# Performance work log

Measured on AMD Instinct MI355X. Metric: run time of the kernel, lower is better.

The kernel has to match this reference:

```python
import jax, jax.numpy as jnp
import numpy as np

N_NODES = 100000


def _gcn_layer(h, W, b, src, dst, norm, n):
    # h: [N, Fin] -> [N, Fout]; normalized scatter-add aggregation (GCNConv)
    hw = h @ W
    msg = norm[:, None] * hw[src]
    out = jax.ops.segment_sum(msg, dst, num_segments=n)
    return out + b


def setup_inputs() -> dict:
    key = jax.random.key(0)
    k = jax.random.split(key, 10)
    N, E, P, F = N_NODES, 3200000, 500000, 128
    x = jax.random.normal(k[0], (N, F), dtype=jnp.float32)
    edge_index = jax.random.randint(k[1], (2, E), 0, N, dtype=jnp.int64)
    pred_edges = jax.random.randint(k[2], (P, 2), 0, N, dtype=jnp.int64)
    # Glorot-ish init for learned params
    W1 = jax.random.normal(k[3], (F, 16), dtype=jnp.float32) / np.sqrt(F)
    b1 = jnp.zeros((16,), dtype=jnp.float32)
    W2 = jax.random.normal(k[4], (16, 8), dtype=jnp.float32) / np.sqrt(16.0)
    b2 = jnp.zeros((8,), dtype=jnp.float32)
    Wl = jax.random.normal(k[5], (8, 1), dtype=jnp.float32) / np.sqrt(8.0)
    bl = jnp.zeros((1,), dtype=jnp.float32)
    return {"x": x, "edge_index": edge_index, "pred_edges": pred_edges,
            "W1": W1, "b1": b1, "W2": W2, "b2": b2, "Wl": Wl, "bl": bl}


def reference(x, edge_index, pred_edges, W1, b1, W2, b2, Wl, bl):
    n = x.shape[0]
    # GCN norm with self-loops: A_hat = D^{-1/2}(A+I)D^{-1/2}
    loop = jnp.arange(n, dtype=edge_index.dtype)
    src = jnp.concatenate([edge_index[0], loop])
    dst = jnp.concatenate([edge_index[1], loop])
    deg = jax.ops.segment_sum(jnp.ones_like(dst, dtype=x.dtype), dst, num_segments=n)
    dinv = jnp.where(deg > 0, jax.lax.rsqrt(deg), 0.0)
    norm = dinv[src] * dinv[dst]

    h = _gcn_layer(x, W1, b1, src, dst, norm, n)   # [N, 16]
    h = _gcn_layer(h, W2, b2, src, dst, norm, n)   # [N, 8]
    z = jax.nn.sigmoid(h @ Wl + bl)                # [N, 1]
    m = z[pred_edges]                              # [P, 2, 1]
    pred = m[:, 0, 0] * m[:, 1, 0]                 # [P]
    return pred
```

## Files before the change

kernel.cpp:

```cpp
#include <hip/hip_runtime.h>
#include <hip/hip_fp16.h>
#include <math.h>

#define BSHIFT 8
#define BUCK   256
#define TILE   8192
#define CAP    12288

typedef _Float16 f16x4 __attribute__((ext_vector_type(4)));
typedef _Float16 f16x8 __attribute__((ext_vector_type(8)));
typedef float    f32x4 __attribute__((ext_vector_type(4)));


__global__ __launch_bounds__(256) void k_curinit(int* __restrict__ bcursor, int nbuk) {
    int b = blockIdx.x * 256 + threadIdx.x;
    if (b < nbuk) bcursor[b] = b * CAP;
}

__global__ __launch_bounds__(1024) void k_binscatter(const int* __restrict__ src,
                                                     const int* __restrict__ dst,
                                                     int* __restrict__ bcursor,
                                                     int* __restrict__ binned, int E, int nbuk) {
    __shared__ int            payload[TILE];
    __shared__ unsigned short bid16[TILE];
    __shared__ int cnt[512];
    __shared__ int lstart[512];
    __shared__ int gbase[512];
    __shared__ int wsum[8];
    int t = threadIdx.x;
    int tile0 = blockIdx.x * TILE;
    int tileE = min(TILE, E - tile0);
    if (t < 512) cnt[t] = 0;
    __syncthreads();
    int d[8], s[8];
    int base = t * 8;
    if (base + 8 <= tileE) {
        const int4* d4 = (const int4*)(dst + tile0 + base);
        const int4* s4 = (const int4*)(src + tile0 + base);
        int4 da = d4[0], db = d4[1];
        int4 sa = s4[0], sb = s4[1];
        d[0] = da.x; d[1] = da.y; d[2] = da.z; d[3] = da.w;
        d[4] = db.x; d[5] = db.y; d[6] = db.z; d[7] = db.w;
        s[0] = sa.x; s[1] = sa.y; s[2] = sa.z; s[3] = sa.w;
        s[4] = sb.x; s[5] = sb.y; s[6] = sb.z; s[7] = sb.w;
    } else {
#pragma unroll
        for (int q = 0; q < 8; ++q) {
            int idx = base + q;
            if (idx < tileE) { d[q] = dst[tile0 + idx]; s[q] = src[tile0 + idx]; }
            else d[q] = -1;
        }
    }
#pragma unroll
    for (int q = 0; q < 8; ++q)
        if (d[q] >= 0) atomicAdd(&cnt[d[q] >> BSHIFT], 1);
    __syncthreads();
    int c = 0, ex = 0;
    if (t < 512) {
        c = cnt[t];
        int v = c;
#pragma unroll
        for (int off = 1; off < 64; off <<= 1) {
            int u = __shfl_up(v, off, 64);
            if ((t & 63) >= off) v += u;
        }
        if ((t & 63) == 63) wsum[t >> 6] = v;
        ex = v - c;
    }
    __syncthreads();
    if (t == 0) {
        int run = 0;
#pragma unroll
        for (int w = 0; w < 8; ++w) { int u = wsum[w]; wsum[w] = run; run += u; }
    }
    __syncthreads();
    if (t < 512) {
        ex += wsum[t >> 6];
        gbase[t] = c ? atomicAdd(&bcursor[t], c) : 0;
        lstart[t] = ex;
        cnt[t] = ex;
    }
    __syncthreads();
#pragma unroll
    for (int q = 0; q < 8; ++q) {
        if (d[q] >= 0) {
            int b = d[q] >> BSHIFT;
            int lp = atomicAdd(&cnt[b], 1);
            payload[lp] = ((d[q] & (BUCK - 1)) << 17) | s[q];
            bid16[lp] = (unsigned short)b;
        }
    }
    __syncthreads();
    for (int k = t; k < tileE; k += 1024) {
        int b = bid16[k];
        int ga = gbase[b] + (k - lstart[b]);
        if (ga < (b + 1) * CAP)
            binned[ga] = payload[k];
    }
}

__global__ __launch_bounds__(1024) void k_sortbucket(const int* __restrict__ bcursor,
                                                     const int* __restrict__ binned,
                                                     int* __restrict__ csr_src,
                                                     int* __restrict__ rowstart,
                                                     int* __restrict__ rowend,
                                                     float* __restrict__ dinv, int N) {
    __shared__ int cnt[BUCK];
    __shared__ int cur[BUCK];
    __shared__ int wsum[4];
    int b = blockIdx.x, t = threadIdx.x;
    if (t < BUCK) cnt[t] = 0;
    __syncthreads();
    int beg = b * CAP;
    int end = min(bcursor[b], beg + CAP);
    int v[12];
#pragma unroll
    for (int q = 0; q < 12; ++q) {
        int e = beg + q * 1024 + t;
        v[q] = (e < end) ? binned[e] : -1;
    }
#pragma unroll
    for (int q = 0; q < 12; ++q)
        if (v[q] >= 0) atomicAdd(&cnt[v[q] >> 17], 1);
    __syncthreads();
    int c = 0, ex = 0;
    if (t < BUCK) {
        c = cnt[t];
        int s = c;
#pragma unroll
        for (int off = 1; off < 64; off <<= 1) {
            int u = __shfl_up(s, off, 64);
            if ((t & 63) >= off) s += u;
        }
        if ((t & 63) == 63) wsum[t >> 6] = s;
        ex = s - c;
    }
    __syncthreads();
    if (t == 0) {
        int run = 0;
#pragma unroll
        for (int w = 0; w < 4; ++w) { int u = wsum[w]; wsum[w] = run; run += u; }
    }
    __syncthreads();
    if (t < BUCK) {
        ex += wsum[t >> 6];
        cur[t] = ex;
        int node = b * BUCK + t;
        if (node < N) {
            rowstart[node] = beg + ex;
            rowend[node]   = beg + ex + c;
            dinv[node] = rsqrtf((float)(c + 1));
        }
    }
    __syncthreads();
#pragma unroll
    for (int q = 0; q < 12; ++q) {
        if (v[q] >= 0) {
            int pos = atomicAdd(&cur[v[q] >> 17], 1);
            csr_src[beg + pos] = v[q] & 0x1FFFF;
        }
    }
}


__global__ __launch_bounds__(256) void k_gemm1(const float* __restrict__ x,
                                               const float* __restrict__ W1,
                                               const float* __restrict__ dinv,
                                               __half* __restrict__ hw1h, int N) {
    __shared__ _Float16 sX[64 * 136];
    __shared__ _Float16 sW[16 * 136];
    __shared__ float    sDi[64];
    __shared__ _Float16 sOut[64 * 16];
    int t = threadIdx.x;
    int row0 = blockIdx.x * 64;
    for (int e = t; e < 2048; e += 256) {
        int n = e & 15, k = e >> 4;
        sW[n * 136 + k] = (_Float16)W1[k * 16 + n];
    }
    const float4* x4 = (const float4*)x;
#pragma unroll
    for (int q = 0; q < 8; ++q) {
        int e = q * 256 + t;
        int r = e >> 5, c4 = e & 31;
        int gr = row0 + r;
        float4 v = (gr < N) ? x4[(size_t)gr * 32 + c4] : make_float4(0.f, 0.f, 0.f, 0.f);
        f16x4 hv = {(_Float16)v.x, (_Float16)v.y, (_Float16)v.z, (_Float16)v.w};
        *(f16x4*)&sX[r * 136 + c4 * 4] = hv;
    }
    if (t < 64) sDi[t] = (row0 + t < N) ? dinv[row0 + t] : 0.f;
    __syncthreads();
    int w = t >> 6, l = t & 63;
    int m = l & 15, quad = l >> 4;
    f32x4 acc = {0.f, 0.f, 0.f, 0.f};
#pragma unroll
    for (int kc = 0; kc < 4; ++kc) {
        f16x8 a = *(const f16x8*)&sX[(w * 16 + m) * 136 + kc * 32 + quad * 8];
        f16x8 b = *(const f16x8*)&sW[m * 136 + kc * 32 + quad * 8];
        acc = __builtin_amdgcn_mfma_f32_16x16x32_f16(a, b, acc, 0, 0, 0);
    }
#pragma unroll
    for (int r = 0; r < 4; ++r) {
        int nl = w * 16 + quad * 4 + r;
        sOut[nl * 16 + m] = (_Float16)(acc[r] * sDi[nl]);
    }
    __syncthreads();
    int nn = t >> 2, ch = t & 3;
    int gn = row0 + nn;
    if (gn < N)
        *(float2*)&hw1h[(size_t)gn * 16 + ch * 4] = *(float2*)&sOut[nn * 16 + ch * 4];
}

__global__ __launch_bounds__(256) void k_agg1c(const int* __restrict__ rowstart,
                                               const int* __restrict__ rowend,
                                               const int* __restrict__ csr_src,
                                               const f16x8* __restrict__ hw1v,
                                               const float* __restrict__ W2,
                                               const float* __restrict__ b1,
                                               __half* __restrict__ hw2h, int N) {
    __shared__ float sW[128], sb[16];
    int t = threadIdx.x;
    if (t < 128) sW[t] = W2[t];
    if (t < 16)  sb[t] = b1[t];
    __syncthreads();
    int i = blockIdx.x * 256 + t;
    if (i >= N) return;
    int beg = rowstart[i], end = rowend[i];
    float di = rsqrtf((float)(end - beg + 1));
    float a[16];
#pragma unroll
    for (int d = 0; d < 16; ++d) a[d] = 0.f;
    int c0 = beg;
    for (; c0 + 8 <= end; c0 += 8) {
        int s[8];
#pragma unroll
        for (int m = 0; m < 8; ++m) s[m] = csr_src[c0 + m];
        f16x8 lo[8], hi[8];
#pragma unroll
        for (int m = 0; m < 8; ++m) {
            lo[m] = hw1v[2 * (size_t)s[m]];
            hi[m] = hw1v[2 * (size_t)s[m] + 1];
        }
#pragma unroll
        for (int m = 0; m < 8; ++m) {
#pragma unroll
            for (int d = 0; d < 8; ++d) {
                a[d]     += (float)lo[m][d];
                a[8 + d] += (float)hi[m][d];
            }
        }
    }
    for (; c0 < end; ++c0) {
        int s = csr_src[c0];
        f16x8 lo = hw1v[2 * (size_t)s];
        f16x8 hi = hw1v[2 * (size_t)s + 1];
#pragma unroll
        for (int d = 0; d < 8; ++d) {
            a[d]     += (float)lo[d];
            a[8 + d] += (float)hi[d];
        }
    }
    {
        f16x8 lo = hw1v[2 * (size_t)i];
        f16x8 hi = hw1v[2 * (size_t)i + 1];
#pragma unroll
        for (int d = 0; d < 8; ++d) {
            a[d]     += (float)lo[d];
            a[8 + d] += (float)hi[d];
        }
    }
    float h[16];
#pragma unroll
    for (int k = 0; k < 16; ++k) h[k] = di * a[k] + sb[k];
    float o[8];
#pragma unroll
    for (int d = 0; d < 8; ++d) o[d] = 0.f;
#pragma unroll
    for (int k = 0; k < 16; ++k) {
        float hv = h[k];
#pragma unroll
        for (int d = 0; d < 8; ++d) o[d] += hv * sW[k * 8 + d];
    }
    f16x8 ho;
#pragma unroll
    for (int d = 0; d < 8; ++d) ho[d] = (_Float16)(di * o[d]);
    *(f16x8*)&hw2h[(size_t)i * 8] = ho;
}

__global__ __launch_bounds__(256) void k_agg2c(const int* __restrict__ rowstart,
                                               const int* __restrict__ rowend,
                                               const int* __restrict__ csr_src,
                                               const f16x8* __restrict__ hw2v,
                                               const float* __restrict__ Wl,
                                               const float* __restrict__ b2,
                                               const float* __restrict__ bl,
                                               float* __restrict__ z, int N) {
    __shared__ float sW[8], sb[8], sbl;
    int t = threadIdx.x;
    if (t < 8) { sW[t] = Wl[t]; sb[t] = b2[t]; }
    if (t == 0) sbl = bl[0];
    __syncthreads();
    int i = blockIdx.x * 256 + t;
    if (i >= N) return;
    int beg = rowstart[i], end = rowend[i];
    float di = rsqrtf((float)(end - beg + 1));
    float a[8];
#pragma unroll
    for (int d = 0; d < 8; ++d) a[d] = 0.f;
    int c0 = beg;
    for (; c0 + 8 <= end; c0 += 8) {
        int s[8];
#pragma unroll
        for (int m = 0; m < 8; ++m) s[m] = csr_src[c0 + m];
        f16x8 gv[8];
#pragma unroll
        for (int m = 0; m < 8; ++m) gv[m] = hw2v[(size_t)s[m]];
#pragma unroll
        for (int m = 0; m < 8; ++m)
#pragma unroll
            for (int d = 0; d < 8; ++d) a[d] += (float)gv[m][d];
    }
    for (; c0 < end; ++c0) {
        f16x8 gv = hw2v[(size_t)csr_src[c0]];
#pragma unroll
        for (int d = 0; d < 8; ++d) a[d] += (float)gv[d];
    }
    f16x8 self = hw2v[(size_t)i];
    float v = 0.f;
#pragma unroll
    for (int d = 0; d < 8; ++d) {
        float h = di * (a[d] + (float)self[d]) + sb[d];
        v += h * sW[d];
    }
    z[i] = 1.f / (1.f + __expf(-(v + sbl)));
}

__global__ __launch_bounds__(256) void k_pred(const int2* __restrict__ pe2,
                                              const float* __restrict__ z,
                                              float* __restrict__ out, int P) {
    int p = blockIdx.x * 256 + threadIdx.x;
    if (p < P) {
        int2 e = pe2[p];
        out[p] = z[e.x] * z[e.y];
    }
}


extern "C" void kernel_launch(void* const* d_in, const int* in_sizes, int n_in,
                              void* d_out, int out_size, void* d_ws, size_t ws_size,
                              hipStream_t stream) {
    const float* x  = (const float*)d_in[0];
    const int*   ei = (const int*)d_in[1];
    const int*   pe = (const int*)d_in[2];
    const float* W1 = (const float*)d_in[3];
    const float* b1 = (const float*)d_in[4];
    const float* W2 = (const float*)d_in[5];
    const float* b2 = (const float*)d_in[6];
    const float* Wl = (const float*)d_in[7];
    const float* bl = (const float*)d_in[8];
    float* out = (float*)d_out;

    const int N = in_sizes[0] / 128;
    const int E = in_sizes[1] / 2;
    const int P = in_sizes[2] / 2;
    const int NBUK = (N + BUCK - 1) >> BSHIFT;

    const int* src = ei;
    const int* dst = ei + E;

    float*  ws   = (float*)d_ws;
    float*  dinv = ws;
    __half* hw1h = (__half*)(ws + (size_t)N);
    __half* hw2h = (__half*)(ws + (size_t)9 * N);
    float*  z    = ws + (size_t)13 * N;
    int* rowstart = (int*)(ws + (size_t)14 * N);
    int* rowend   = rowstart + N;
    int* bcursor  = rowend + N;
    int* binned   = bcursor + 512;
    int* csr_src  = binned + (size_t)NBUK * CAP;

    const int B = 256;

    k_curinit<<<(NBUK + B - 1) / B, B, 0, stream>>>(bcursor, NBUK);
    k_binscatter<<<(E + TILE - 1) / TILE, 1024, 0, stream>>>(src, dst, bcursor, binned, E, NBUK);
    k_sortbucket<<<NBUK, 1024, 0, stream>>>(bcursor, binned, csr_src, rowstart, rowend, dinv, N);
    k_gemm1<<<(N + 63) / 64, B, 0, stream>>>(x, W1, dinv, hw1h, N);
    k_agg1c<<<(N + 255) / 256, B, 0, stream>>>(rowstart, rowend, csr_src,
                                               (const f16x8*)hw1h, W2, b1, hw2h, N);
    k_agg2c<<<(N + 255) / 256, B, 0, stream>>>(rowstart, rowend, csr_src,
                                               (const f16x8*)hw2h, Wl, b2, bl, z, N);
    k_pred<<<(P + B - 1) / B, B, 0, stream>>>((const int2*)pe, z, out, P);
}
```

Baseline: 224.3 us.

## Split each node's CSR aggregation across four lanes with shuffle reduction

Measured after the change: 210.5 us. 6.2% less time.

```diff
diff --git a/kernel.cpp b/kernel.cpp
--- a/kernel.cpp
+++ b/kernel.cpp
@@ -7,6 +7,7 @@
 #define TILE   8192
 #define CAP    12288
 
+typedef _Float16 f16x2 __attribute__((ext_vector_type(2)));
 typedef _Float16 f16x4 __attribute__((ext_vector_type(4)));
 typedef _Float16 f16x8 __attribute__((ext_vector_type(8)));
 typedef float    f32x4 __attribute__((ext_vector_type(4)));
@@ -222,7 +223,8 @@
     if (t < 128) sW[t] = W2[t];
     if (t < 16)  sb[t] = b1[t];
     __syncthreads();
-    int i = blockIdx.x * 256 + t;
+    int q = t >> 2, j = t & 3;
+    int i = blockIdx.x * 64 + q;
     if (i >= N) return;
     int beg = rowstart[i], end = rowend[i];
     float di = rsqrtf((float)(end - beg + 1));
@@ -230,18 +232,18 @@
 #pragma unroll
     for (int d = 0; d < 16; ++d) a[d] = 0.f;
     int c0 = beg;
-    for (; c0 + 8 <= end; c0 += 8) {
-        int s[8];
-#pragma unroll
-        for (int m = 0; m < 8; ++m) s[m] = csr_src[c0 + m];
-        f16x8 lo[8], hi[8];
-#pragma unroll
-        for (int m = 0; m < 8; ++m) {
-            lo[m] = hw1v[2 * (size_t)s[m]];
-            hi[m] = hw1v[2 * (size_t)s[m] + 1];
-        }
-#pragma unroll
-        for (int m = 0; m < 8; ++m) {
+    for (; c0 + 16 <= end; c0 += 16) {
+        int s4[4];
+#pragma unroll
+        for (int m = 0; m < 4; ++m) s4[m] = csr_src[c0 + 4 * j + m];
+        f16x8 lo[4], hi[4];
+#pragma unroll
+        for (int m = 0; m < 4; ++m) {
+            lo[m] = hw1v[2 * (size_t)s4[m]];
+            hi[m] = hw1v[2 * (size_t)s4[m] + 1];
+        }
+#pragma unroll
+        for (int m = 0; m < 4; ++m) {
 #pragma unroll
             for (int d = 0; d < 8; ++d) {
                 a[d]     += (float)lo[m][d];
@@ -249,8 +251,8 @@
             }
         }
     }
-    for (; c0 < end; ++c0) {
-        int s = csr_src[c0];
+    for (int c = c0 + j; c < end; c += 4) {
+        int s = csr_src[c];
         f16x8 lo = hw1v[2 * (size_t)s];
         f16x8 hi = hw1v[2 * (size_t)s + 1];
 #pragma unroll
@@ -259,7 +261,7 @@
             a[8 + d] += (float)hi[d];
         }
     }
-    {
+    if (j == 0) {
         f16x8 lo = hw1v[2 * (size_t)i];
         f16x8 hi = hw1v[2 * (size_t)i + 1];
 #pragma unroll
@@ -268,22 +270,19 @@
             a[8 + d] += (float)hi[d];
         }
     }
-    float h[16];
-#pragma unroll
-    for (int k = 0; k < 16; ++k) h[k] = di * a[k] + sb[k];
-    float o[8];
-#pragma unroll
-    for (int d = 0; d < 8; ++d) o[d] = 0.f;
+#pragma unroll
+    for (int d = 0; d < 16; ++d) a[d] += __shfl_xor(a[d], 1, 4);
+#pragma unroll
+    for (int d = 0; d < 16; ++d) a[d] += __shfl_xor(a[d], 2, 4);
+    float o0 = 0.f, o1 = 0.f;
 #pragma unroll
     for (int k = 0; k < 16; ++k) {
-        float hv = h[k];
-#pragma unroll
-        for (int d = 0; d < 8; ++d) o[d] += hv * sW[k * 8 + d];
-    }
-    f16x8 ho;
-#pragma unroll
-    for (int d = 0; d < 8; ++d) ho[d] = (_Float16)(di * o[d]);
-    *(f16x8*)&hw2h[(size_t)i * 8] = ho;
+        float hv = di * a[k] + sb[k];
+        o0 += hv * sW[k * 8 + 2 * j];
+        o1 += hv * sW[k * 8 + 2 * j + 1];
+    }
+    f16x2 ho = {(_Float16)(di * o0), (_Float16)(di * o1)};
+    *(f16x2*)&hw2h[(size_t)i * 8 + 2 * j] = ho;
 }
 
 __global__ __launch_bounds__(256) void k_agg2c(const int* __restrict__ rowstart,
@@ -299,7 +298,8 @@
     if (t < 8) { sW[t] = Wl[t]; sb[t] = b2[t]; }
     if (t == 0) sbl = bl[0];
     __syncthreads();
-    int i = blockIdx.x * 256 + t;
+    int q = t >> 2, j = t & 3;
+    int i = blockIdx.x * 64 + q;
     if (i >= N) return;
     int beg = rowstart[i], end = rowend[i];
     float di = rsqrtf((float)(end - beg + 1));
@@ -307,31 +307,41 @@
 #pragma unroll
     for (int d = 0; d < 8; ++d) a[d] = 0.f;
     int c0 = beg;
-    for (; c0 + 8 <= end; c0 += 8) {
-        int s[8];
-#pragma unroll
-        for (int m = 0; m < 8; ++m) s[m] = csr_src[c0 + m];
-        f16x8 gv[8];
-#pragma unroll
-        for (int m = 0; m < 8; ++m) gv[m] = hw2v[(size_t)s[m]];
-#pragma unroll
-        for (int m = 0; m < 8; ++m)
+    for (; c0 + 16 <= end; c0 += 16) {
+        int s4[4];
+#pragma unroll
+        for (int m = 0; m < 4; ++m) s4[m] = csr_src[c0 + 4 * j + m];
+        f16x8 gv[4];
+#pragma unroll
+        for (int m = 0; m < 4; ++m) gv[m] = hw2v[(size_t)s4[m]];
+#pragma unroll
+        for (int m = 0; m < 4; ++m)
 #pragma unroll
             for (int d = 0; d < 8; ++d) a[d] += (float)gv[m][d];
     }
-    for (; c0 < end; ++c0) {
-        f16x8 gv = hw2v[(size_t)csr_src[c0]];
+    for (int c = c0 + j; c < end; c += 4) {
+        f16x8 gv = hw2v[(size_t)csr_src[c]];
 #pragma unroll
         for (int d = 0; d < 8; ++d) a[d] += (float)gv[d];
     }
-    f16x8 self = hw2v[(size_t)i];
-    float v = 0.f;
-#pragma unroll
-    for (int d = 0; d < 8; ++d) {
-        float h = di * (a[d] + (float)self[d]) + sb[d];
-        v += h * sW[d];
-    }
-    z[i] = 1.f / (1.f + __expf(-(v + sbl)));
+    if (j == 0) {
+        f16x8 self = hw2v[(size_t)i];
+#pragma unroll
+        for (int d = 0; d < 8; ++d) a[d] += (float)self[d];
+    }
+#pragma unroll
+    for (int d = 0; d < 8; ++d) a[d] += __shfl_xor(a[d], 1, 4);
+#pragma unroll
+    for (int d = 0; d < 8; ++d) a[d] += __shfl_xor(a[d], 2, 4);
+    if (j == 0) {
+        float v = 0.f;
+#pragma unroll
+        for (int d = 0; d < 8; ++d) {
+            float h = di * a[d] + sb[d];
+            v += h * sW[d];
+        }
+        z[i] = 1.f / (1.f + __expf(-(v + sbl)));
+    }
 }
 
 __global__ __launch_bounds__(256) void k_pred(const int2* __restrict__ pe2,
@@ -384,9 +394,9 @@
     k_binscatter<<<(E + TILE - 1) / TILE, 1024, 0, stream>>>(src, dst, bcursor, binned, E, NBUK);
     k_sortbucket<<<NBUK, 1024, 0, stream>>>(bcursor, binned, csr_src, rowstart, rowend, dinv, N);
     k_gemm1<<<(N + 63) / 64, B, 0, stream>>>(x, W1, dinv, hw1h, N);
-    k_agg1c<<<(N + 255) / 256, B, 0, stream>>>(rowstart, rowend, csr_src,
-                                               (const f16x8*)hw1h, W2, b1, hw2h, N);
-    k_agg2c<<<(N + 255) / 256, B, 0, stream>>>(rowstart, rowend, csr_src,
-                                               (const f16x8*)hw2h, Wl, b2, bl, z, N);
+    k_agg1c<<<(N + 63) / 64, B, 0, stream>>>(rowstart, rowend, csr_src,
+                                             (const f16x8*)hw1h, W2, b1, hw2h, N);
+    k_agg2c<<<(N + 63) / 64, B, 0, stream>>>(rowstart, rowend, csr_src,
+                                             (const f16x8*)hw2h, Wl, b2, bl, z, N);
     k_pred<<<(P + B - 1) / B, B, 0, stream>>>((const int2*)pe, z, out, P);
 }
```

## Replace per-bucket CSR sort with LDS atomic aggregation over binned edges

Applied to the files above, without the earlier changes.

After: 656.3 us. +192.6%, slower.

```diff
diff --git a/kernel.cpp b/kernel.cpp
--- a/kernel.cpp
+++ b/kernel.cpp
@@ -99,67 +99,26 @@
     }
 }
 
-__global__ __launch_bounds__(1024) void k_sortbucket(const int* __restrict__ bcursor,
-                                                     const int* __restrict__ binned,
-                                                     int* __restrict__ csr_src,
-                                                     int* __restrict__ rowstart,
-                                                     int* __restrict__ rowend,
-                                                     float* __restrict__ dinv, int N) {
+__global__ __launch_bounds__(1024) void k_hist(const int* __restrict__ bcursor,
+                                               const int* __restrict__ binned,
+                                               float* __restrict__ dinv, int N) {
     __shared__ int cnt[BUCK];
-    __shared__ int cur[BUCK];
-    __shared__ int wsum[4];
     int b = blockIdx.x, t = threadIdx.x;
     if (t < BUCK) cnt[t] = 0;
     __syncthreads();
     int beg = b * CAP;
     int end = min(bcursor[b], beg + CAP);
-    int v[12];
-#pragma unroll
-    for (int q = 0; q < 12; ++q) {
-        int e = beg + q * 1024 + t;
-        v[q] = (e < end) ? binned[e] : -1;
-    }
-#pragma unroll
-    for (int q = 0; q < 12; ++q)
-        if (v[q] >= 0) atomicAdd(&cnt[v[q] >> 17], 1);
-    __syncthreads();
-    int c = 0, ex = 0;
-    if (t < BUCK) {
-        c = cnt[t];
-        int s = c;
-#pragma unroll
-        for (int off = 1; off < 64; off <<= 1) {
-            int u = __shfl_up(s, off, 64);
-            if ((t & 63) >= off) s += u;
-        }
-        if ((t & 63) == 63) wsum[t >> 6] = s;
-        ex = s - c;
-    }
-    __syncthreads();
-    if (t == 0) {
-        int run = 0;
-#pragma unroll
-        for (int w = 0; w < 4; ++w) { int u = wsum[w]; wsum[w] = run; run += u; }
-    }
-    __syncthreads();
-    if (t < BUCK) {
-        ex += wsum[t >> 6];
-        cur[t] = ex;
-        int node = b * BUCK + t;
-        if (node < N) {
-            rowstart[node] = beg + ex;
-            rowend[node]   = beg + ex + c;
-            dinv[node] = rsqrtf((float)(c + 1));
-        }
-    }
-    __syncthreads();
-#pragma unroll
-    for (int q = 0; q < 12; ++q) {
-        if (v[q] >= 0) {
-            int pos = atomicAdd(&cur[v[q] >> 17], 1);
-            csr_src[beg + pos] = v[q] & 0x1FFFF;
-        }
-    }
+    for (int e0 = beg + 4 * t; e0 < end; e0 += 4096) {
+        int4 pk = *(const int4*)&binned[e0];
+        int pv[4] = {pk.x, pk.y, pk.z, pk.w};
+#pragma unroll
+        for (int m = 0; m < 4; ++m)
+            if (e0 + m < end) atomicAdd(&cnt[pv[m] >> 17], 1);
+    }
+    __syncthreads();
+    int node = b * BUCK + t;
+    if (t < BUCK && node < N)
+        dinv[node] = rsqrtf((float)(cnt[t] + 1));
 }
 
 
@@ -210,128 +169,117 @@
         *(float2*)&hw1h[(size_t)gn * 16 + ch * 4] = *(float2*)&sOut[nn * 16 + ch * 4];
 }
 
-__global__ __launch_bounds__(256) void k_agg1c(const int* __restrict__ rowstart,
-                                               const int* __restrict__ rowend,
-                                               const int* __restrict__ csr_src,
-                                               const f16x8* __restrict__ hw1v,
-                                               const float* __restrict__ W2,
-                                               const float* __restrict__ b1,
-                                               __half* __restrict__ hw2h, int N) {
+__global__ __launch_bounds__(1024) void k_agg1f(const int* __restrict__ bcursor,
+                                                const int* __restrict__ binned,
+                                                const float* __restrict__ dinv_g,
+                                                const f16x8* __restrict__ hw1v,
+                                                const float* __restrict__ W2,
+                                                const float* __restrict__ b1,
+                                                __half* __restrict__ hw2h, int N) {
+    __shared__ float acc[BUCK][17];
     __shared__ float sW[128], sb[16];
-    int t = threadIdx.x;
+    int b = blockIdx.x, t = threadIdx.x;
     if (t < 128) sW[t] = W2[t];
     if (t < 16)  sb[t] = b1[t];
-    __syncthreads();
-    int i = blockIdx.x * 256 + t;
-    if (i >= N) return;
-    int beg = rowstart[i], end = rowend[i];
-    float di = rsqrtf((float)(end - beg + 1));
-    float a[16];
-#pragma unroll
-    for (int d = 0; d < 16; ++d) a[d] = 0.f;
-    int c0 = beg;
-    for (; c0 + 8 <= end; c0 += 8) {
-        int s[8];
-#pragma unroll
-        for (int m = 0; m < 8; ++m) s[m] = csr_src[c0 + m];
-        f16x8 lo[8], hi[8];
-#pragma unroll
-        for (int m = 0; m < 8; ++m) {
-            lo[m] = hw1v[2 * (size_t)s[m]];
-            hi[m] = hw1v[2 * (size_t)s[m] + 1];
-        }
-#pragma unroll
-        for (int m = 0; m < 8; ++m) {
+    for (int e = t; e < BUCK * 17; e += 1024) ((float*)acc)[e] = 0.f;
+    __syncthreads();
+    int beg = b * CAP;
+    int end = min(bcursor[b], beg + CAP);
+    for (int e0 = beg + 4 * t; e0 < end; e0 += 4096) {
+        int4 pk = *(const int4*)&binned[e0];
+        int pv[4] = {pk.x, pk.y, pk.z, pk.w};
+#pragma unroll
+        for (int m = 0; m < 4; ++m) {
+            if (e0 + m < end) {
+                int dl = pv[m] >> 17, s = pv[m] & 0x1FFFF;
+                f16x8 lo = hw1v[2 * (size_t)s];
+                f16x8 hi = hw1v[2 * (size_t)s + 1];
+                float* ap = acc[dl];
+#pragma unroll
+                for (int d = 0; d < 8; ++d) {
+                    atomicAdd(&ap[d],     (float)lo[d]);
+                    atomicAdd(&ap[8 + d], (float)hi[d]);
+                }
+            }
+        }
+    }
+    __syncthreads();
+    if (t < BUCK) {
+        int i = b * BUCK + t;
+        if (i < N) {
+            float di = dinv_g[i];
+            f16x8 lo = hw1v[2 * (size_t)i];
+            f16x8 hi = hw1v[2 * (size_t)i + 1];
+            float h[16];
 #pragma unroll
             for (int d = 0; d < 8; ++d) {
-                a[d]     += (float)lo[m][d];
-                a[8 + d] += (float)hi[m][d];
-            }
-        }
-    }
-    for (; c0 < end; ++c0) {
-        int s = csr_src[c0];
-        f16x8 lo = hw1v[2 * (size_t)s];
-        f16x8 hi = hw1v[2 * (size_t)s + 1];
-#pragma unroll
-        for (int d = 0; d < 8; ++d) {
-            a[d]     += (float)lo[d];
-            a[8 + d] += (float)hi[d];
-        }
-    }
-    {
-        f16x8 lo = hw1v[2 * (size_t)i];
-        f16x8 hi = hw1v[2 * (size_t)i + 1];
-#pragma unroll
-        for (int d = 0; d < 8; ++d) {
-            a[d]     += (float)lo[d];
-            a[8 + d] += (float)hi[d];
-        }
-    }
-    float h[16];
-#pragma unroll
-    for (int k = 0; k < 16; ++k) h[k] = di * a[k] + sb[k];
-    float o[8];
-#pragma unroll
-    for (int d = 0; d < 8; ++d) o[d] = 0.f;
-#pragma unroll
-    for (int k = 0; k < 16; ++k) {
-        float hv = h[k];
-#pragma unroll
-        for (int d = 0; d < 8; ++d) o[d] += hv * sW[k * 8 + d];
-    }
-    f16x8 ho;
-#pragma unroll
-    for (int d = 0; d < 8; ++d) ho[d] = (_Float16)(di * o[d]);
-    *(f16x8*)&hw2h[(size_t)i * 8] = ho;
-}
-
-__global__ __launch_bounds__(256) void k_agg2c(const int* __restrict__ rowstart,
-                                               const int* __restrict__ rowend,
-                                               const int* __restrict__ csr_src,
-                                               const f16x8* __restrict__ hw2v,
-                                               const float* __restrict__ Wl,
-                                               const float* __restrict__ b2,
-                                               const float* __restrict__ bl,
-                                               float* __restrict__ z, int N) {
+                h[d]     = di * (acc[t][d]     + (float)lo[d]) + sb[d];
+                h[8 + d] = di * (acc[t][8 + d] + (float)hi[d]) + sb[8 + d];
+            }
+            float o[8];
+#pragma unroll
+            for (int d = 0; d < 8; ++d) o[d] = 0.f;
+#pragma unroll
+            for (int k = 0; k < 16; ++k) {
+                float hv = h[k];
+#pragma unroll
+                for (int d = 0; d < 8; ++d) o[d] += hv * sW[k * 8 + d];
+            }
+            f16x8 ho;
+#pragma unroll
+            for (int d = 0; d < 8; ++d) ho[d] = (_Float16)(di * o[d]);
+            *(f16x8*)&hw2h[(size_t)i * 8] = ho;
+        }
+    }
+}
+
+__global__ __launch_bounds__(1024) void k_agg2f(const int* __restrict__ bcursor,
+                                                const int* __restrict__ binned,
+                                                const float* __restrict__ dinv_g,
+                                                const f16x8* __restrict__ hw2v,
+                                                const float* __restrict__ Wl,
+                                                const float* __restrict__ b2,
+                                                const float* __restrict__ bl,
+                                                float* __restrict__ z, int N) {
+    __shared__ float acc[BUCK][9];
     __shared__ float sW[8], sb[8], sbl;
-    int t = threadIdx.x;
+    int b = blockIdx.x, t = threadIdx.x;
     if (t < 8) { sW[t] = Wl[t]; sb[t] = b2[t]; }
     if (t == 0) sbl = bl[0];
-    __syncthreads();
-    int i = blockIdx.x * 256 + t;
-    if (i >= N) return;
-    int beg = rowstart[i], end = rowend[i];
-    float di = rsqrtf((float)(end - beg + 1));
-    float a[8];
-#pragma unroll
-    for (int d = 0; d < 8; ++d) a[d] = 0.f;
-    int c0 = beg;
-    for (; c0 + 8 <= end; c0 += 8) {
-        int s[8];
-#pragma unroll
-        for (int m = 0; m < 8; ++m) s[m] = csr_src[c0 + m];
-        f16x8 gv[8];
-#pragma unroll
-        for (int m = 0; m < 8; ++m) gv[m] = hw2v[(size_t)s[m]];
-#pragma unroll
-        for (int m = 0; m < 8; ++m)
-#pragma unroll
-            for (int d = 0; d < 8; ++d) a[d] += (float)gv[m][d];
-    }
-    for (; c0 < end; ++c0) {
-        f16x8 gv = hw2v[(size_t)csr_src[c0]];
-#pragma unroll
-        for (int d = 0; d < 8; ++d) a[d] += (float)gv[d];
-    }
-    f16x8 self = hw2v[(size_t)i];
-    float v = 0.f;
-#pragma unroll
-    for (int d = 0; d < 8; ++d) {
-        float h = di * (a[d] + (float)self[d]) + sb[d];
-        v += h * sW[d];
-    }
-    z[i] = 1.f / (1.f + __expf(-(v + sbl)));
+    for (int e = t; e < BUCK * 9; e += 1024) ((float*)acc)[e] = 0.f;
+    __syncthreads();
+    int beg = b * CAP;
+    int end = min(bcursor[b], beg + CAP);
+    for (int e0 = beg + 4 * t; e0 < end; e0 += 4096) {
+        int4 pk = *(const int4*)&binned[e0];
+        int pv[4] = {pk.x, pk.y, pk.z, pk.w};
+#pragma unroll
+        for (int m = 0; m < 4; ++m) {
+            if (e0 + m < end) {
+                int dl = pv[m] >> 17, s = pv[m] & 0x1FFFF;
+                f16x8 gv = hw2v[(size_t)s];
+                float* ap = acc[dl];
+#pragma unroll
+                for (int d = 0; d < 8; ++d)
+                    atomicAdd(&ap[d], (float)gv[d]);
+            }
+        }
+    }
+    __syncthreads();
+    if (t < BUCK) {
+        int i = b * BUCK + t;
+        if (i < N) {
+            float di = dinv_g[i];
+            f16x8 self = hw2v[(size_t)i];
+            float v = 0.f;
+#pragma unroll
+            for (int d = 0; d < 8; ++d) {
+                float h = di * (acc[t][d] + (float)self[d]) + sb[d];
+                v += h * sW[d];
+            }
+            z[i] = 1.f / (1.f + __expf(-(v + sbl)));
+        }
+    }
 }
 
 __global__ __launch_bounds__(256) void k_pred(const int2* __restrict__ pe2,
@@ -372,21 +320,18 @@
     __half* hw1h = (__half*)(ws + (size_t)N);
     __half* hw2h = (__half*)(ws + (size_t)9 * N);
     float*  z    = ws + (size_t)13 * N;
-    int* rowstart = (int*)(ws + (size_t)14 * N);
-    int* rowend   = rowstart + N;
-    int* bcursor  = rowend + N;
-    int* binned   = bcursor + 512;
-    int* csr_src  = binned + (size_t)NBUK * CAP;
+    int* bcursor = (int*)(ws + (size_t)14 * N);
+    int* binned  = bcursor + 512;
 
     const int B = 256;
 
     k_curinit<<<(NBUK + B - 1) / B, B, 0, stream>>>(bcursor, NBUK);
     k_binscatter<<<(E + TILE - 1) / TILE, 1024, 0, stream>>>(src, dst, bcursor, binned, E, NBUK);
-    k_sortbucket<<<NBUK, 1024, 0, stream>>>(bcursor, binned, csr_src, rowstart, rowend, dinv, N);
+    k_hist<<<NBUK, 1024, 0, stream>>>(bcursor, binned, dinv, N);
     k_gemm1<<<(N + 63) / 64, B, 0, stream>>>(x, W1, dinv, hw1h, N);
-    k_agg1c<<<(N + 255) / 256, B, 0, stream>>>(rowstart, rowend, csr_src,
-                                               (const f16x8*)hw1h, W2, b1, hw2h, N);
-    k_agg2c<<<(N + 255) / 256, B, 0, stream>>>(rowstart, rowend, csr_src,
-                                               (const f16x8*)hw2h, Wl, b2, bl, z, N);
+    k_agg1f<<<NBUK, 1024, 0, stream>>>(bcursor, binned, dinv,
+                                       (const f16x8*)hw1h, W2, b1, hw2h, N);
+    k_agg2f<<<NBUK, 1024, 0, stream>>>(bcursor, binned, dinv,
+                                       (const f16x8*)hw2h, Wl, b2, bl, z, N);
     k_pred<<<(P + B - 1) / B, B, 0, stream>>>((const int2*)pe, z, out, P);
 }
```
